# Performance work log

Hardware: AMD Instinct MI355X
Metric: run time of the kernel (lower is better)

Reference implementation:

```python
import jax, jax.numpy as jnp
import numpy as np

DIM = 1024
HEADS = 16
DIM_HEAD = 64
NUM_KV_HEADS = 4
INNER = HEADS * DIM_HEAD          # 1024
KV_DIM = NUM_KV_HEADS * DIM_HEAD  # 256
SCALE = DIM_HEAD ** -0.5


def setup_inputs() -> dict:
    key = jax.random.key(0)
    ks = jax.random.split(key, 7)
    B, S = 2, 2048
    x = jax.random.normal(ks[0], (B, S, DIM), dtype=jnp.float32)
    init = lambda k, shape: jax.random.normal(k, shape, dtype=jnp.float32) * (shape[0] ** -0.5)
    return {
        "x": x,
        "ln_gamma": jnp.ones((DIM,), jnp.float32),
        "ln_beta": jnp.zeros((DIM,), jnp.float32),
        "w_q": init(ks[1], (DIM, INNER)),
        "w_k": init(ks[2], (DIM, KV_DIM)),
        "w_v": init(ks[3], (DIM, KV_DIM)),
        "w_o": init(ks[4], (INNER, DIM)),
        "b_o": jnp.zeros((DIM,), jnp.float32),
    }


def reference(x, ln_gamma, ln_beta, w_q, w_k, w_v, w_o, b_o):
    B, S, _ = x.shape
    g, hpg, d = NUM_KV_HEADS, HEADS // NUM_KV_HEADS, DIM_HEAD
    # LayerNorm (eps matches torch default 1e-5)
    mu = jnp.mean(x, axis=-1, keepdims=True)
    var = jnp.mean((x - mu) ** 2, axis=-1, keepdims=True)
    xn = (x - mu) * jax.lax.rsqrt(var + 1e-5) * ln_gamma + ln_beta
    # projections
    q = xn @ w_q  # [B,S,INNER]
    k = xn @ w_k  # [B,S,KV_DIM]
    v = xn @ w_v
    # q: b s (g hpg d) -> b g hpg s d  (head index h = g*hpg + i, g-major)
    q = q.reshape(B, S, g, hpg, d).transpose(0, 2, 3, 1, 4)
    k = k.reshape(B, S, g, d).transpose(0, 2, 1, 3)  # [B,g,S,d]
    v = v.reshape(B, S, g, d).transpose(0, 2, 1, 3)
    dots = jnp.einsum('bghqd,bgkd->bghqk', q, k) * SCALE
    attn = jax.nn.softmax(dots, axis=-1)
    out = jnp.einsum('bghqk,bgkd->bghqd', attn, v)
    # b g hpg s d -> b s (g hpg d)
    out = out.transpose(0, 3, 1, 2, 4).reshape(B, S, INNER)
    return out @ w_o + b_o
```

## Files before the change

kernel.cpp:

```cpp
#include <hip/hip_runtime.h>

typedef unsigned short u16;
typedef __bf16 bf16x8 __attribute__((ext_vector_type(8)));
typedef __bf16 bf16x2 __attribute__((ext_vector_type(2)));
typedef short s16x4 __attribute__((ext_vector_type(4)));
typedef float f32x4 __attribute__((ext_vector_type(4)));

__device__ __forceinline__ u16 f32_to_bf16(float f) {
  union { float f; unsigned u; } v; v.f = f;
  unsigned r = v.u + 0x7FFFu + ((v.u >> 16) & 1u);
  return (u16)(r >> 16);
}
__device__ __forceinline__ unsigned f2u(float f) { union { float f; unsigned u; } v; v.f = f; return v.u; }

__device__ __forceinline__ unsigned pack2bf16(float a, float b) {
#if __has_builtin(__builtin_amdgcn_cvt_pk_bf16_f32)
  bf16x2 r = __builtin_amdgcn_cvt_pk_bf16_f32(a, b);
  return *(unsigned*)&r;
#else
  return (f2u(a) >> 16) | (f2u(b) & 0xFFFF0000u);
#endif
}

__global__ __launch_bounds__(256) void transpose_cvt_multi(
    const float* __restrict__ w_q, const float* __restrict__ w_k,
    const float* __restrict__ w_v, const float* __restrict__ w_o,
    u16* __restrict__ wqkvT, u16* __restrict__ woT) {
  const float* src; u16* dst; int N;
  switch (blockIdx.z) {
    case 0: src = w_q; dst = wqkvT; N = 1024; break;
    case 1: src = w_k; dst = wqkvT + 1024 * 1024; N = 256; break;
    case 2: src = w_v; dst = wqkvT + 1280 * 1024; N = 256; break;
    default: src = w_o; dst = woT; N = 1024; break;
  }
  int n0 = blockIdx.x * 64;
  if (n0 >= N) return;
  const int K = 1024;
  __shared__ float tile[64][65];
  int k0 = blockIdx.y * 64;
  int t = threadIdx.x;
  int c = t & 63, r4 = t >> 6;
#pragma unroll
  for (int rr = r4; rr < 64; rr += 4)
    tile[rr][c] = src[(size_t)(k0 + rr) * N + n0 + c];
  __syncthreads();
#pragma unroll
  for (int rr = r4; rr < 64; rr += 4)
    dst[(size_t)(n0 + rr) * K + k0 + c] = f32_to_bf16(tile[c][rr]);
}

__global__ __launch_bounds__(256) void ln_kernel(
    const float* __restrict__ x, const float* __restrict__ gamma,
    const float* __restrict__ beta, u16* __restrict__ xn) {
  int row = blockIdx.x;
  int t = threadIdx.x;
  const float4 v = ((const float4*)(x + (size_t)row * 1024))[t];
  float s = v.x + v.y + v.z + v.w;
  float ss = v.x * v.x + v.y * v.y + v.z * v.z + v.w * v.w;
#pragma unroll
  for (int m = 1; m < 64; m <<= 1) {
    s += __shfl_xor(s, m, 64);
    ss += __shfl_xor(ss, m, 64);
  }
  __shared__ float as_[4], ass[4];
  int wave = t >> 6;
  if ((t & 63) == 0) { as_[wave] = s; ass[wave] = ss; }
  __syncthreads();
  s = as_[0] + as_[1] + as_[2] + as_[3];
  ss = ass[0] + ass[1] + ass[2] + ass[3];
  float mu = s * (1.0f / 1024.0f);
  float var = ss * (1.0f / 1024.0f) - mu * mu;
  float rstd = rsqrtf(var + 1e-5f);
  float4 g = ((const float4*)gamma)[t];
  float4 b = ((const float4*)beta)[t];
  uint2 o;
  o.x = pack2bf16((v.x - mu) * rstd * g.x + b.x, (v.y - mu) * rstd * g.y + b.y);
  o.y = pack2bf16((v.z - mu) * rstd * g.z + b.z, (v.w - mu) * rstd * g.w + b.w);
  ((uint2*)(xn + (size_t)row * 1024))[t] = o;
}

template <int OUT_MODE>
__global__ __launch_bounds__(256) void gemm_bf16_k(
    const u16* __restrict__ A, const u16* __restrict__ Bt,
    void* __restrict__ Cv, const float* __restrict__ bias,
    int M, int N, int K, int ldc, float qscale, int qcols) {
  __shared__ __align__(16) u16 sA[128 * 72];
  __shared__ __align__(16) u16 sB[128 * 72];
  int t = threadIdx.x;
  int m0 = blockIdx.y * 128, n0 = blockIdx.x * 128;
  int wave = t >> 6, lane = t & 63;
  int wm = wave >> 1, wn = wave & 1;
  int l15 = lane & 15, quad = lane >> 4;

  f32x4 acc[4][4];
#pragma unroll
  for (int i = 0; i < 4; i++)
#pragma unroll
    for (int j = 0; j < 4; j++) acc[i][j] = f32x4{0.f, 0.f, 0.f, 0.f};

  int r = t >> 3, q = t & 7;
  const u16* Ap = A + (size_t)(m0 + r) * K + q * 8;
  const u16* Bp = Bt + (size_t)(n0 + r) * K + q * 8;

  for (int k0 = 0; k0 < K; k0 += 64) {
    uint4 av0 = *(const uint4*)(Ap + k0);
    uint4 av1 = *(const uint4*)(Ap + k0 + (size_t)32 * K);
    uint4 av2 = *(const uint4*)(Ap + k0 + (size_t)64 * K);
    uint4 av3 = *(const uint4*)(Ap + k0 + (size_t)96 * K);
    uint4 bv0 = *(const uint4*)(Bp + k0);
    uint4 bv1 = *(const uint4*)(Bp + k0 + (size_t)32 * K);
    uint4 bv2 = *(const uint4*)(Bp + k0 + (size_t)64 * K);
    uint4 bv3 = *(const uint4*)(Bp + k0 + (size_t)96 * K);
    __syncthreads();
    *(uint4*)&sA[(r) * 72 + q * 8] = av0;
    *(uint4*)&sA[(r + 32) * 72 + q * 8] = av1;
    *(uint4*)&sA[(r + 64) * 72 + q * 8] = av2;
    *(uint4*)&sA[(r + 96) * 72 + q * 8] = av3;
    *(uint4*)&sB[(r) * 72 + q * 8] = bv0;
    *(uint4*)&sB[(r + 32) * 72 + q * 8] = bv1;
    *(uint4*)&sB[(r + 64) * 72 + q * 8] = bv2;
    *(uint4*)&sB[(r + 96) * 72 + q * 8] = bv3;
    __syncthreads();
#pragma unroll
    for (int ks = 0; ks < 2; ++ks) {
      bf16x8 af[4], bf[4];
#pragma unroll
      for (int mi = 0; mi < 4; mi++)
        af[mi] = *(const bf16x8*)&sA[(wm * 64 + mi * 16 + l15) * 72 + ks * 32 + quad * 8];
#pragma unroll
      for (int ni = 0; ni < 4; ni++)
        bf[ni] = *(const bf16x8*)&sB[(wn * 64 + ni * 16 + l15) * 72 + ks * 32 + quad * 8];
#pragma unroll
      for (int mi = 0; mi < 4; mi++)
#pragma unroll
        for (int ni = 0; ni < 4; ni++)
          acc[mi][ni] = __builtin_amdgcn_mfma_f32_16x16x32_bf16(
              af[mi], bf[ni], acc[mi][ni], 0, 0, 0);
    }
  }
#pragma unroll
  for (int mi = 0; mi < 4; mi++)
#pragma unroll
    for (int ni = 0; ni < 4; ni++) {
      int row = m0 + wm * 64 + mi * 16 + quad * 4;
      int col = n0 + wn * 64 + ni * 16 + l15;
#pragma unroll
      for (int rr = 0; rr < 4; rr++) {
        float vv = acc[mi][ni][rr];
        if (OUT_MODE == 0) {
          float sc = (col < qcols) ? qscale : 1.0f;
          ((u16*)Cv)[(size_t)(row + rr) * ldc + col] = f32_to_bf16(vv * sc);
        } else {
          ((float*)Cv)[(size_t)(row + rr) * ldc + col] = vv + bias[col];
        }
      }
    }
}

__global__ __launch_bounds__(256) void attn_kernel(
    const u16* __restrict__ qkv, u16* __restrict__ attn_out) {
  const int LD = 1536;
  int qt = blockIdx.x;
  int bh = blockIdx.y;
  int b = bh >> 4, h = bh & 15, g = h >> 2;

  __shared__ __align__(16) u16 sK[64 * 72];
  __shared__ __align__(16) u16 sV[64 * 72];

  int t = threadIdx.x, wave = t >> 6, lane = t & 63;
  int l15 = lane & 15, quad = lane >> 4;

  const u16* qbase = qkv + (size_t)(b * 2048 + qt * 256 + wave * 64) * LD + h * 64;
  const u16* kbase = qkv + (size_t)(b * 2048) * LD + 1024 + g * 64;
  const u16* vbase = kbase + 256;

  bf16x8 qf[4][2];
#pragma unroll
  for (int qs = 0; qs < 4; ++qs)
#pragma unroll
    for (int ks = 0; ks < 2; ++ks)
      qf[qs][ks] = *(const bf16x8*)(qbase + (size_t)(qs * 16 + l15) * LD + ks * 32 + quad * 8);

  f32x4 oacc[4][4];
  f32x4 lacc[4];
#pragma unroll
  for (int qs = 0; qs < 4; ++qs) {
    lacc[qs] = f32x4{0.f, 0.f, 0.f, 0.f};
#pragma unroll
    for (int md = 0; md < 4; ++md) oacc[qs][md] = f32x4{0.f, 0.f, 0.f, 0.f};
  }

  const s16x4 ones = {(short)0x3F80, (short)0x3F80, (short)0x3F80, (short)0x3F80};
  const f32x4 fzero = {0.f, 0.f, 0.f, 0.f};

  int sr = t >> 3, sq = t & 7;
  int vkp = (t & 31) * 2, vdc = (t >> 5) * 8;

  uint4 ka0, ka1, va0, va1;
  {
    const u16* kp0 = kbase + (size_t)sr * LD + sq * 8;
    ka0 = *(const uint4*)kp0;
    ka1 = *(const uint4*)(kp0 + (size_t)32 * LD);
    const u16* vp0 = vbase + (size_t)vkp * LD + vdc;
    va0 = *(const uint4*)vp0;
    va1 = *(const uint4*)(vp0 + LD);
  }

  for (int kt = 0; kt < 32; ++kt) {
    __syncthreads();
    *(uint4*)&sK[sr * 72 + sq * 8] = ka0;
    *(uint4*)&sK[(sr + 32) * 72 + sq * 8] = ka1;
    {
      const unsigned* aw = (const unsigned*)&va0;
      const unsigned* bw = (const unsigned*)&va1;
#pragma unroll
      for (int w = 0; w < 4; ++w) {
        unsigned lo = (aw[w] & 0xFFFFu) | (bw[w] << 16);
        unsigned hi = (aw[w] >> 16) | (bw[w] & 0xFFFF0000u);
        *(unsigned*)&sV[(vdc + 2 * w) * 72 + vkp] = lo;
        *(unsigned*)&sV[(vdc + 2 * w + 1) * 72 + vkp] = hi;
      }
    }
    __syncthreads();

    if (kt < 31) {
      const u16* kp0 = kbase + (size_t)((kt + 1) * 64 + sr) * LD + sq * 8;
      ka0 = *(const uint4*)kp0;
      ka1 = *(const uint4*)(kp0 + (size_t)32 * LD);
      const u16* vp0 = vbase + (size_t)((kt + 1) * 64 + vkp) * LD + vdc;
      va0 = *(const uint4*)vp0;
      va1 = *(const uint4*)(vp0 + LD);
    }

    s16x4 pf[4][4];
#pragma unroll
    for (int ni = 0; ni < 4; ++ni) {
      bf16x8 kf0 = *(const bf16x8*)&sK[(ni * 16 + l15) * 72 + quad * 8];
      bf16x8 kf1 = *(const bf16x8*)&sK[(ni * 16 + l15) * 72 + 32 + quad * 8];
      f32x4 sacc[4];
#pragma unroll
      for (int qs = 0; qs < 4; ++qs)
        sacc[qs] = __builtin_amdgcn_mfma_f32_16x16x32_bf16(kf0, qf[qs][0], fzero, 0, 0, 0);
#pragma unroll
      for (int qs = 0; qs < 4; ++qs)
        sacc[qs] = __builtin_amdgcn_mfma_f32_16x16x32_bf16(kf1, qf[qs][1], sacc[qs], 0, 0, 0);
#pragma unroll
      for (int qs = 0; qs < 4; ++qs) {
        float p0 = __builtin_amdgcn_exp2f(sacc[qs][0]);
        float p1 = __builtin_amdgcn_exp2f(sacc[qs][1]);
        float p2 = __builtin_amdgcn_exp2f(sacc[qs][2]);
        float p3 = __builtin_amdgcn_exp2f(sacc[qs][3]);
        uint2 pk;
        pk.x = pack2bf16(p0, p1);
        pk.y = pack2bf16(p2, p3);
        pf[qs][ni] = *(s16x4*)&pk;
        lacc[qs] = __builtin_amdgcn_mfma_f32_16x16x16bf16_1k(ones, pf[qs][ni], lacc[qs], 0, 0, 0);
      }
    }

#pragma unroll
    for (int md = 0; md < 4; ++md)
#pragma unroll
      for (int ni = 0; ni < 4; ++ni) {
        s16x4 vf = *(const s16x4*)&sV[(md * 16 + l15) * 72 + ni * 16 + quad * 4];
#pragma unroll
        for (int qs = 0; qs < 4; ++qs)
          oacc[qs][md] = __builtin_amdgcn_mfma_f32_16x16x16bf16_1k(vf, pf[qs][ni], oacc[qs][md], 0, 0, 0);
      }
  }

#pragma unroll
  for (int qs = 0; qs < 4; ++qs) {
    float rinv = 1.0f / lacc[qs][0];
    u16* obase = attn_out +
                 (size_t)(b * 2048 + qt * 256 + wave * 64 + qs * 16 + l15) * 1024 +
                 h * 64 + quad * 4;
#pragma unroll
    for (int md = 0; md < 4; ++md) {
      uint2 o;
      o.x = pack2bf16(oacc[qs][md][0] * rinv, oacc[qs][md][1] * rinv);
      o.y = pack2bf16(oacc[qs][md][2] * rinv, oacc[qs][md][3] * rinv);
      *(uint2*)(obase + md * 16) = o;
    }
  }
}

extern "C" void kernel_launch(void* const* d_in, const int* in_sizes, int n_in,
                              void* d_out, int out_size, void* d_ws, size_t ws_size,
                              hipStream_t stream) {
  const float* x = (const float*)d_in[0];
  const float* gamma = (const float*)d_in[1];
  const float* beta = (const float*)d_in[2];
  const float* w_q = (const float*)d_in[3];
  const float* w_k = (const float*)d_in[4];
  const float* w_v = (const float*)d_in[5];
  const float* w_o = (const float*)d_in[6];
  const float* b_o = (const float*)d_in[7];
  float* out = (float*)d_out;

  char* ws = (char*)d_ws;
  u16* wqkvT = (u16*)ws;
  u16* woT = (u16*)(ws + 3u * 1024 * 1024);
  u16* xn = (u16*)(ws + 5u * 1024 * 1024);
  u16* qkv = (u16*)(ws + 13u * 1024 * 1024);
  u16* attn = (u16*)(ws + 25u * 1024 * 1024);

  const float cexp = 0.125f * 1.44269504088896f;

  transpose_cvt_multi<<<dim3(16, 16, 4), 256, 0, stream>>>(w_q, w_k, w_v, w_o,
                                                           wqkvT, woT);
  ln_kernel<<<4096, 256, 0, stream>>>(x, gamma, beta, xn);

  gemm_bf16_k<0><<<dim3(12, 32), 256, 0, stream>>>(xn, wqkvT, qkv, nullptr,
                                                   4096, 1536, 1024, 1536,
                                                   cexp, 1024);

  attn_kernel<<<dim3(8, 32), 256, 0, stream>>>(qkv, attn);

  gemm_bf16_k<1><<<dim3(8, 32), 256, 0, stream>>>(attn, woT, out, b_o,
                                                  4096, 1024, 1024, 1024,
                                                  1.0f, 0);
}
```

Baseline: 206.9 us.

## Split attention over two KV halves with combine pass; shrink GEMM M-tile to 64

Attention is split along the key dimension into two halves (blockIdx.z), each writing unnormalized bf16 partial outputs and row sums, and a new combine kernel adds them and normalizes. Because the kernel subtracts no running max, the two halves combine by plain addition. This doubles the attention grid from 256 to 512 blocks to fill more CUs, at the cost of an extra pass over the partials and bf16 rounding of unnormalized sums. The GEMMs also drop to a 64-row M tile, doubling their block count. P packing switches to truncation via perm, and the V transpose uses perm instructions.

```diff
diff --git a/kernel.cpp b/kernel.cpp
--- a/kernel.cpp
+++ b/kernel.cpp
@@ -2,23 +2,41 @@
 
 typedef unsigned short u16;
 typedef __bf16 bf16x8 __attribute__((ext_vector_type(8)));
-typedef __bf16 bf16x2 __attribute__((ext_vector_type(2)));
 typedef short s16x4 __attribute__((ext_vector_type(4)));
 typedef float f32x4 __attribute__((ext_vector_type(4)));
 
+__device__ __forceinline__ unsigned f2u(float f) { union { float f; unsigned u; } v; v.f = f; return v.u; }
+__device__ __forceinline__ float u2f(unsigned u) { union { unsigned u; float f; } v; v.u = u; return v.f; }
+
 __device__ __forceinline__ u16 f32_to_bf16(float f) {
-  union { float f; unsigned u; } v; v.f = f;
-  unsigned r = v.u + 0x7FFFu + ((v.u >> 16) & 1u);
-  return (u16)(r >> 16);
-}
-__device__ __forceinline__ unsigned f2u(float f) { union { float f; unsigned u; } v; v.f = f; return v.u; }
-
-__device__ __forceinline__ unsigned pack2bf16(float a, float b) {
-#if __has_builtin(__builtin_amdgcn_cvt_pk_bf16_f32)
-  bf16x2 r = __builtin_amdgcn_cvt_pk_bf16_f32(a, b);
-  return *(unsigned*)&r;
+  unsigned u = f2u(f);
+  return (u16)((u + 0x7FFFu + ((u >> 16) & 1u)) >> 16);
+}
+__device__ __forceinline__ unsigned pack_rnd(float a, float b) {
+  unsigned ra = f2u(a), rb = f2u(b);
+  ra = ra + 0x7FFFu + ((ra >> 16) & 1u);
+  rb = (rb + 0x7FFFu + ((rb >> 16) & 1u)) & 0xFFFF0000u;
+  return (ra >> 16) | rb;
+}
+__device__ __forceinline__ unsigned pack_trunc(float a, float b) {
+#if __has_builtin(__builtin_amdgcn_perm)
+  return __builtin_amdgcn_perm(f2u(b), f2u(a), 0x07060302u);
 #else
   return (f2u(a) >> 16) | (f2u(b) & 0xFFFF0000u);
+#endif
+}
+__device__ __forceinline__ unsigned perm_lo(unsigned a, unsigned b) {
+#if __has_builtin(__builtin_amdgcn_perm)
+  return __builtin_amdgcn_perm(b, a, 0x05040100u);
+#else
+  return (a & 0xFFFFu) | (b << 16);
+#endif
+}
+__device__ __forceinline__ unsigned perm_hi(unsigned a, unsigned b) {
+#if __has_builtin(__builtin_amdgcn_perm)
+  return __builtin_amdgcn_perm(b, a, 0x07060302u);
+#else
+  return (a >> 16) | (b & 0xFFFF0000u);
 #endif
 }
 
@@ -74,8 +92,8 @@
   float4 g = ((const float4*)gamma)[t];
   float4 b = ((const float4*)beta)[t];
   uint2 o;
-  o.x = pack2bf16((v.x - mu) * rstd * g.x + b.x, (v.y - mu) * rstd * g.y + b.y);
-  o.y = pack2bf16((v.z - mu) * rstd * g.z + b.z, (v.w - mu) * rstd * g.w + b.w);
+  o.x = pack_rnd((v.x - mu) * rstd * g.x + b.x, (v.y - mu) * rstd * g.y + b.y);
+  o.y = pack_rnd((v.z - mu) * rstd * g.z + b.z, (v.w - mu) * rstd * g.w + b.w);
   ((uint2*)(xn + (size_t)row * 1024))[t] = o;
 }
 
@@ -84,17 +102,17 @@
     const u16* __restrict__ A, const u16* __restrict__ Bt,
     void* __restrict__ Cv, const float* __restrict__ bias,
     int M, int N, int K, int ldc, float qscale, int qcols) {
-  __shared__ __align__(16) u16 sA[128 * 72];
+  __shared__ __align__(16) u16 sA[64 * 72];
   __shared__ __align__(16) u16 sB[128 * 72];
   int t = threadIdx.x;
-  int m0 = blockIdx.y * 128, n0 = blockIdx.x * 128;
+  int m0 = blockIdx.y * 64, n0 = blockIdx.x * 128;
   int wave = t >> 6, lane = t & 63;
   int wm = wave >> 1, wn = wave & 1;
   int l15 = lane & 15, quad = lane >> 4;
 
-  f32x4 acc[4][4];
-#pragma unroll
-  for (int i = 0; i < 4; i++)
+  f32x4 acc[2][4];
+#pragma unroll
+  for (int i = 0; i < 2; i++)
 #pragma unroll
     for (int j = 0; j < 4; j++) acc[i][j] = f32x4{0.f, 0.f, 0.f, 0.f};
 
@@ -105,8 +123,6 @@
   for (int k0 = 0; k0 < K; k0 += 64) {
     uint4 av0 = *(const uint4*)(Ap + k0);
     uint4 av1 = *(const uint4*)(Ap + k0 + (size_t)32 * K);
-    uint4 av2 = *(const uint4*)(Ap + k0 + (size_t)64 * K);
-    uint4 av3 = *(const uint4*)(Ap + k0 + (size_t)96 * K);
     uint4 bv0 = *(const uint4*)(Bp + k0);
     uint4 bv1 = *(const uint4*)(Bp + k0 + (size_t)32 * K);
     uint4 bv2 = *(const uint4*)(Bp + k0 + (size_t)64 * K);
@@ -114,8 +130,6 @@
     __syncthreads();
     *(uint4*)&sA[(r) * 72 + q * 8] = av0;
     *(uint4*)&sA[(r + 32) * 72 + q * 8] = av1;
-    *(uint4*)&sA[(r + 64) * 72 + q * 8] = av2;
-    *(uint4*)&sA[(r + 96) * 72 + q * 8] = av3;
     *(uint4*)&sB[(r) * 72 + q * 8] = bv0;
     *(uint4*)&sB[(r + 32) * 72 + q * 8] = bv1;
     *(uint4*)&sB[(r + 64) * 72 + q * 8] = bv2;
@@ -123,15 +137,15 @@
     __syncthreads();
 #pragma unroll
     for (int ks = 0; ks < 2; ++ks) {
-      bf16x8 af[4], bf[4];
-#pragma unroll
-      for (int mi = 0; mi < 4; mi++)
-        af[mi] = *(const bf16x8*)&sA[(wm * 64 + mi * 16 + l15) * 72 + ks * 32 + quad * 8];
+      bf16x8 af[2], bf[4];
+#pragma unroll
+      for (int mi = 0; mi < 2; mi++)
+        af[mi] = *(const bf16x8*)&sA[(wm * 32 + mi * 16 + l15) * 72 + ks * 32 + quad * 8];
 #pragma unroll
       for (int ni = 0; ni < 4; ni++)
         bf[ni] = *(const bf16x8*)&sB[(wn * 64 + ni * 16 + l15) * 72 + ks * 32 + quad * 8];
 #pragma unroll
-      for (int mi = 0; mi < 4; mi++)
+      for (int mi = 0; mi < 2; mi++)
 #pragma unroll
         for (int ni = 0; ni < 4; ni++)
           acc[mi][ni] = __builtin_amdgcn_mfma_f32_16x16x32_bf16(
@@ -139,10 +153,10 @@
     }
   }
 #pragma unroll
-  for (int mi = 0; mi < 4; mi++)
+  for (int mi = 0; mi < 2; mi++)
 #pragma unroll
     for (int ni = 0; ni < 4; ni++) {
-      int row = m0 + wm * 64 + mi * 16 + quad * 4;
+      int row = m0 + wm * 32 + mi * 16 + quad * 4;
       int col = n0 + wn * 64 + ni * 16 + l15;
 #pragma unroll
       for (int rr = 0; rr < 4; rr++) {
@@ -158,11 +172,15 @@
 }
 
 __global__ __launch_bounds__(256) void attn_kernel(
-    const u16* __restrict__ qkv, u16* __restrict__ attn_out) {
+    const u16* __restrict__ qkv, u16* __restrict__ oP0, u16* __restrict__ oP1,
+    float* __restrict__ lP0, float* __restrict__ lP1) {
   const int LD = 1536;
   int qt = blockIdx.x;
   int bh = blockIdx.y;
+  int kz = blockIdx.z;
   int b = bh >> 4, h = bh & 15, g = h >> 2;
+  u16* oP = kz ? oP1 : oP0;
+  float* lP = kz ? lP1 : lP0;
 
   __shared__ __align__(16) u16 sK[64 * 72];
   __shared__ __align__(16) u16 sV[64 * 72];
@@ -171,7 +189,7 @@
   int l15 = lane & 15, quad = lane >> 4;
 
   const u16* qbase = qkv + (size_t)(b * 2048 + qt * 256 + wave * 64) * LD + h * 64;
-  const u16* kbase = qkv + (size_t)(b * 2048) * LD + 1024 + g * 64;
+  const u16* kbase = qkv + (size_t)(b * 2048 + kz * 1024) * LD + 1024 + g * 64;
   const u16* vbase = kbase + 256;
 
   bf16x8 qf[4][2];
@@ -206,7 +224,7 @@
     va1 = *(const uint4*)(vp0 + LD);
   }
 
-  for (int kt = 0; kt < 32; ++kt) {
+  for (int kt = 0; kt < 16; ++kt) {
     __syncthreads();
     *(uint4*)&sK[sr * 72 + sq * 8] = ka0;
     *(uint4*)&sK[(sr + 32) * 72 + sq * 8] = ka1;
@@ -215,15 +233,13 @@
       const unsigned* bw = (const unsigned*)&va1;
 #pragma unroll
       for (int w = 0; w < 4; ++w) {
-        unsigned lo = (aw[w] & 0xFFFFu) | (bw[w] << 16);
-        unsigned hi = (aw[w] >> 16) | (bw[w] & 0xFFFF0000u);
-        *(unsigned*)&sV[(vdc + 2 * w) * 72 + vkp] = lo;
-        *(unsigned*)&sV[(vdc + 2 * w + 1) * 72 + vkp] = hi;
+        *(unsigned*)&sV[(vdc + 2 * w) * 72 + vkp] = perm_lo(aw[w], bw[w]);
+        *(unsigned*)&sV[(vdc + 2 * w + 1) * 72 + vkp] = perm_hi(aw[w], bw[w]);
       }
     }
     __syncthreads();
 
-    if (kt < 31) {
+    if (kt < 15) {
       const u16* kp0 = kbase + (size_t)((kt + 1) * 64 + sr) * LD + sq * 8;
       ka0 = *(const uint4*)kp0;
       ka1 = *(const uint4*)(kp0 + (size_t)32 * LD);
@@ -251,8 +267,8 @@
         float p2 = __builtin_amdgcn_exp2f(sacc[qs][2]);
         float p3 = __builtin_amdgcn_exp2f(sacc[qs][3]);
         uint2 pk;
-        pk.x = pack2bf16(p0, p1);
-        pk.y = pack2bf16(p2, p3);
+        pk.x = pack_trunc(p0, p1);
+        pk.y = pack_trunc(p2, p3);
         pf[qs][ni] = *(s16x4*)&pk;
         lacc[qs] = __builtin_amdgcn_mfma_f32_16x16x16bf16_1k(ones, pf[qs][ni], lacc[qs], 0, 0, 0);
       }
@@ -271,18 +287,42 @@
 
 #pragma unroll
   for (int qs = 0; qs < 4; ++qs) {
-    float rinv = 1.0f / lacc[qs][0];
-    u16* obase = attn_out +
-                 (size_t)(b * 2048 + qt * 256 + wave * 64 + qs * 16 + l15) * 1024 +
-                 h * 64 + quad * 4;
+    int row = b * 2048 + qt * 256 + wave * 64 + qs * 16 + l15;
+    u16* ob = oP + (size_t)row * 1024 + h * 64 + quad * 4;
 #pragma unroll
     for (int md = 0; md < 4; ++md) {
       uint2 o;
-      o.x = pack2bf16(oacc[qs][md][0] * rinv, oacc[qs][md][1] * rinv);
-      o.y = pack2bf16(oacc[qs][md][2] * rinv, oacc[qs][md][3] * rinv);
-      *(uint2*)(obase + md * 16) = o;
-    }
-  }
+      o.x = pack_rnd(oacc[qs][md][0], oacc[qs][md][1]);
+      o.y = pack_rnd(oacc[qs][md][2], oacc[qs][md][3]);
+      *(uint2*)(ob + md * 16) = o;
+    }
+    if (quad == 0) lP[row * 16 + h] = lacc[qs][0];
+  }
+}
+
+__global__ __launch_bounds__(256) void attn_combine(
+    const u16* __restrict__ oP0, u16* __restrict__ oP1_attn,
+    const float* __restrict__ lP0, const float* __restrict__ lP1) {
+  int t = threadIdx.x;
+  int row = blockIdx.x * 2 + (t >> 7);
+  int c8 = (t & 127) * 8;
+  int h = c8 >> 6;
+  float l = lP0[row * 16 + h] + lP1[row * 16 + h];
+  float rinv = 1.0f / l;
+  size_t off = (size_t)row * 1024 + c8;
+  uint4 a = *(const uint4*)(oP0 + off);
+  uint4 bb = *(const uint4*)(oP1_attn + off);
+  const unsigned* aw = (const unsigned*)&a;
+  const unsigned* bw = (const unsigned*)&bb;
+  uint4 o;
+  unsigned* ow = (unsigned*)&o;
+#pragma unroll
+  for (int i = 0; i < 4; ++i) {
+    float x0 = u2f(aw[i] << 16) + u2f(bw[i] << 16);
+    float x1 = u2f(aw[i] & 0xFFFF0000u) + u2f(bw[i] & 0xFFFF0000u);
+    ow[i] = pack_rnd(x0 * rinv, x1 * rinv);
+  }
+  *(uint4*)(oP1_attn + off) = o;
 }
 
 extern "C" void kernel_launch(void* const* d_in, const int* in_sizes, int n_in,
@@ -300,10 +340,13 @@
 
   char* ws = (char*)d_ws;
   u16* wqkvT = (u16*)ws;
+  float* lP0 = (float*)ws;
+  float* lP1 = (float*)(ws + 256u * 1024);
   u16* woT = (u16*)(ws + 3u * 1024 * 1024);
   u16* xn = (u16*)(ws + 5u * 1024 * 1024);
+  u16* oP0 = xn;
   u16* qkv = (u16*)(ws + 13u * 1024 * 1024);
-  u16* attn = (u16*)(ws + 25u * 1024 * 1024);
+  u16* oP1 = (u16*)(ws + 25u * 1024 * 1024);
 
   const float cexp = 0.125f * 1.44269504088896f;
 
@@ -311,13 +354,14 @@
                                                            wqkvT, woT);
   ln_kernel<<<4096, 256, 0, stream>>>(x, gamma, beta, xn);
 
-  gemm_bf16_k<0><<<dim3(12, 32), 256, 0, stream>>>(xn, wqkvT, qkv, nullptr,
+  gemm_bf16_k<0><<<dim3(12, 64), 256, 0, stream>>>(xn, wqkvT, qkv, nullptr,
                                                    4096, 1536, 1024, 1536,
                                                    cexp, 1024);
 
-  attn_kernel<<<dim3(8, 32), 256, 0, stream>>>(qkv, attn);
-
-  gemm_bf16_k<1><<<dim3(8, 32), 256, 0, stream>>>(attn, woT, out, b_o,
+  attn_kernel<<<dim3(8, 32, 2), 256, 0, stream>>>(qkv, oP0, oP1, lP0, lP1);
+  attn_combine<<<dim3(2048), 256, 0, stream>>>(oP0, oP1, lP0, lP1);
+
+  gemm_bf16_k<1><<<dim3(8, 64), 256, 0, stream>>>(oP1, woT, out, b_o,
                                                   4096, 1024, 1024, 1024,
                                                   1.0f, 0);
 }
```

After: 187.3 us. 1.1x faster.
